# Performance work log

Measured on AMD Instinct MI355X. Metric: run time of the kernel, lower is better.

## Reference

```python
import jax, jax.numpy as jnp
from jax import lax
import numpy as np

# pywt sym4 analysis filters (pywt.Wavelet('sym4').dec_lo / .dec_hi)
DEC_LO = np.array([-0.07576571478927333, -0.02963552764599851, 0.49761866763201545,
                   0.8037387518059161, 0.29785779560527736, -0.09921954357684722,
                   -0.012603967262037833, 0.0322231006040427], dtype=np.float32)
DEC_HI = np.array([-0.0322231006040427, -0.012603967262037833, 0.09921954357684722,
                   0.29785779560527736, -0.8037387518059161, 0.49761866763201545,
                   0.02963552764599851, -0.07576571478927333], dtype=np.float32)
L = 8            # sym4 filter length
LEVEL = 4
THRESH = 10.0


def _conv1d(x, kernel, stride, pad):
    # x: (B, T), kernel: (L,) used in correlation sense by lax.conv
    y = lax.conv_general_dilated(x[:, None, :], kernel[None, None, :],
                                 window_strides=(stride,), padding=[pad],
                                 dimension_numbers=('NCH', 'OIH', 'NCH'))
    return y[:, 0, :]


def _dwt1(x, filt):
    # pywt single-level DWT, mode='symmetric':
    #   pad L-1 each side (half-sample symmetric), true convolution, take odd-index
    #   outputs of the 'valid' part -> length floor((N+L-1)/2)
    ext = jnp.pad(x, ((0, 0), (L - 1, L - 1)), mode='symmetric')[:, 1:]
    return _conv1d(ext, filt[::-1], 2, (0, 0))  # flip -> true convolution


def _idwt1(cA, cD, lo, hi):
    # pywt single-level IDWT: upsample by 2, full-convolve with rec filters, sum,
    # trim L-2 from the left, output length 2*n - L + 2.
    B, n = cA.shape
    upA = jnp.zeros((B, 2 * n), cA.dtype).at[:, ::2].set(cA)
    upD = jnp.zeros((B, 2 * n), cD.dtype).at[:, ::2].set(cD)
    # rec_lo = dec_lo[::-1]; full conv w/ rec_lo == correlation w/ dec_lo
    y = _conv1d(upA, lo, 1, (L - 1, L - 1)) + _conv1d(upD, hi, 1, (L - 1, L - 1))
    return y[:, L - 2: L - 2 + 2 * n - L + 2]


def _wavelet_denoise(x):
    lo = jnp.asarray(DEC_LO)
    hi = jnp.asarray(DEC_HI)
    a = x
    details = []
    for _ in range(LEVEL):
        details.append(_dwt1(a, hi))
        a = _dwt1(a, lo)
    # hard threshold: KEEP coefficients with |c| <= threshold, zero the rest
    details = [jnp.where(jnp.abs(d) <= THRESH, d, jnp.zeros_like(d)) for d in details]
    rec = a
    for d in reversed(details):
        if rec.shape[1] > d.shape[1]:     # pywt waverec a[:-1] trim
            rec = rec[:, :d.shape[1]]
        rec = _idwt1(rec, d, lo, hi)
    return rec


def setup_inputs() -> dict:
    key = jax.random.key(0)
    k1, k2 = jax.random.split(key)
    x = jax.random.normal(k1, (100000, 512), dtype=jnp.float32) * 20.0
    edge_index = jax.random.randint(k2, (2, 100000), 0, 100000, dtype=jnp.int64)
    return {"x": x, "edge_index": edge_index, "num_nodes": 100000}


def reference(x, edge_index, num_nodes):
    # edge_index / num_nodes are unused by the original forward
    return _wavelet_denoise(x)
```

## Files before the change

### kernel.cpp

```cpp
#include <hip/hip_runtime.h>
#include <cstddef>

#define THRESH_V 10.0f
#define RPB 4
#define SLICE 1040

static __device__ __forceinline__ void wave_sync() {
  asm volatile("s_waitcnt lgkmcnt(0)" ::: "memory");
}

#define RLO0 ( 0.0322231006040427f)
#define RLO1 (-0.012603967262037833f)
#define RLO2 (-0.09921954357684722f)
#define RLO3 ( 0.29785779560527736f)
#define RLO4 ( 0.8037387518059161f)
#define RLO5 ( 0.49761866763201545f)
#define RLO6 (-0.02963552764599851f)
#define RLO7 (-0.07576571478927333f)
#define RHI0 (-0.07576571478927333f)
#define RHI1 ( 0.02963552764599851f)
#define RHI2 ( 0.49761866763201545f)
#define RHI3 (-0.8037387518059161f)
#define RHI4 ( 0.29785779560527736f)
#define RHI5 ( 0.09921954357684722f)
#define RHI6 (-0.012603967262037833f)
#define RHI7 (-0.0322231006040427f)

static __device__ __forceinline__ float2 fwd_core(float v0, float v1, float v2,
                                                  float v3, float v4, float v5,
                                                  float v6, float v7) {
#pragma clang fp contract(off)
  float pl0 = v0 * RLO0, pl1 = v1 * RLO1, pl2 = v2 * RLO2, pl3 = v3 * RLO3;
  float pl4 = v4 * RLO4, pl5 = v5 * RLO5, pl6 = v6 * RLO6, pl7 = v7 * RLO7;
  float ph0 = v0 * RHI0, ph1 = v1 * RHI1, ph2 = v2 * RHI2, ph3 = v3 * RHI3;
  float ph4 = v4 * RHI4, ph5 = v5 * RHI5, ph6 = v6 * RHI6, ph7 = v7 * RHI7;
  float sLo = ((pl0 + pl1) + (pl2 + pl3)) + ((pl4 + pl5) + (pl6 + pl7));
  float sHi = ((ph0 + ph1) + (ph2 + ph3)) + ((ph4 + ph5) + (ph6 + ph7));
  return make_float2(sLo, sHi);
}

static __device__ __forceinline__ float symget(const float* E, const float* O,
                                               int k, int n) {
  int idx = (k < 0) ? (-1 - k) : ((k >= n) ? (2 * n - 1 - k) : k);
  return (idx & 1) ? O[idx >> 1] : E[idx >> 1];
}

template <bool SPLIT_OUT>
static __device__ __forceinline__ void fwd_stage(const float* __restrict__ E,
                                                 const float* __restrict__ O,
                                                 int n,
                                                 float* __restrict__ caE,
                                                 float* __restrict__ caO,
                                                 float* __restrict__ cd,
                                                 int lane) {
  const int m = (n + 7) >> 1;
  const int iMax = (n - 2) >> 1;

  for (int i = 3 + lane; i <= iMax; i += 64) {
    const float* e = E + (i - 3);
    const float* o = O + (i - 3);
    float2 s = fwd_core(e[0], o[0], e[1], o[1], e[2], o[2], e[3], o[3]);
    if constexpr (SPLIT_OUT) {
      float* dst = (i & 1) ? caO : caE;
      dst[i >> 1] = s.x;
    } else {
      caE[i] = s.x;
    }
    cd[i] = (fabsf(s.y) <= THRESH_V) ? s.y : 0.f;
  }

  int bi = -1;
  if (lane < 3) bi = lane;
  else if (lane >= 4 && lane < 8) {
    const int t = lane - 4;
    if (t < m - 1 - iMax) bi = iMax + 1 + t;
  }
  if (bi >= 0) {
    float v[8];
#pragma unroll
    for (int t = 0; t < 8; ++t) v[t] = symget(E, O, 2 * bi - 6 + t, n);
    float2 s = fwd_core(v[0], v[1], v[2], v[3], v[4], v[5], v[6], v[7]);
    if constexpr (SPLIT_OUT) {
      float* dst = (bi & 1) ? caO : caE;
      dst[bi >> 1] = s.x;
    } else {
      caE[bi] = s.x;
    }
    cd[bi] = (fabsf(s.y) <= THRESH_V) ? s.y : 0.f;
  }
}

static __device__ __forceinline__ void inv_stage(const float* __restrict__ ca,
                                                 const float* __restrict__ cd,
                                                 float* __restrict__ dst,
                                                 int outLen, int lane) {
  const int pairs = (outLen + 1) >> 1;
  for (int t = lane; t < pairs; t += 64) {
    float a0 = ca[t], a1 = ca[t + 1], a2 = ca[t + 2], a3 = ca[t + 3];
    float e0 = cd[t], e1 = cd[t + 1], e2 = cd[t + 2], e3 = cd[t + 3];
    float se = fmaf(a0, -0.02963552764599851f,
               fmaf(a1,  0.8037387518059161f,
               fmaf(a2, -0.09921954357684722f, a3 *  0.0322231006040427f)))
             + fmaf(e0, -0.012603967262037833f,
               fmaf(e1,  0.29785779560527736f,
               fmaf(e2,  0.49761866763201545f, e3 * -0.07576571478927333f)));
    float so = fmaf(a0, -0.07576571478927333f,
               fmaf(a1,  0.49761866763201545f,
               fmaf(a2,  0.29785779560527736f, a3 * -0.012603967262037833f)))
             + fmaf(e0, -0.0322231006040427f,
               fmaf(e1,  0.09921954357684722f,
               fmaf(e2, -0.8037387518059161f,  e3 *  0.02963552764599851f)));
    const int q = 2 * t;
    if (q + 1 < outLen) {
      *reinterpret_cast<float2*>(dst + q) = make_float2(se, so);
    } else {
      dst[q] = se;
    }
  }
}

__global__ __launch_bounds__(256, 8) void wavelet_denoise_kernel(
    const float* __restrict__ x, float* __restrict__ out, int nrows) {
  __shared__ float lds[RPB][SLICE];
  const int wave = threadIdx.x >> 6;
  const int lane = threadIdx.x & 63;
  const int row = blockIdx.x * RPB + wave;
  if (row >= nrows) return;

  float* S = lds[wave];
  float* sxE  = S;
  float* sxO  = S + 256;
  float* ca1E = S + 512;
  float* ca1O = S + 642;
  float* d1   = S + 772;
  float* ca2E = S + 0;
  float* ca2O = S + 67;
  float* d2   = S + 133;
  float* ca3E = S + 266;
  float* ca3O = S + 301;
  float* d3   = S + 336;
  float* ca4  = S + 406;
  float* d4   = S + 444;
  float* rec70  = S + 512;
  float* rec133 = S + 0;
  float* rec259 = S + 512;

  {
    const float4* src4 = reinterpret_cast<const float4*>(x + (size_t)row * 512);
    float2* dE = reinterpret_cast<float2*>(sxE);
    float2* dO = reinterpret_cast<float2*>(sxO);
    for (int c = lane; c < 128; c += 64) {
      float4 v = src4[c];
      dE[c] = make_float2(v.x, v.z);
      dO[c] = make_float2(v.y, v.w);
    }
  }
  wave_sync();

  fwd_stage<true >(sxE,  sxO,  512, ca1E, ca1O,   d1, lane); wave_sync();
  fwd_stage<true >(ca1E, ca1O, 259, ca2E, ca2O,   d2, lane); wave_sync();
  fwd_stage<true >(ca2E, ca2O, 133, ca3E, ca3O,   d3, lane); wave_sync();
  fwd_stage<false>(ca3E, ca3O,  70, ca4,  nullptr, d4, lane); wave_sync();

  inv_stage(ca4,    d4, rec70,   70, lane); wave_sync();
  inv_stage(rec70,  d3, rec133, 133, lane); wave_sync();
  inv_stage(rec133, d2, rec259, 259, lane); wave_sync();
  inv_stage(rec259, d1, out + (size_t)row * 512, 512, lane);
}

extern "C" void kernel_launch(void* const* d_in, const int* in_sizes, int n_in,
                              void* d_out, int out_size, void* d_ws, size_t ws_size,
                              hipStream_t stream) {
  const float* x = (const float*)d_in[0];
  float* out = (float*)d_out;
  const int nrows = in_sizes[0] / 512;
  const int grid = (nrows + RPB - 1) / RPB;
  wavelet_denoise_kernel<<<dim3(grid), dim3(256), 0, stream>>>(x, out, nrows);
}
```

Baseline: 382.7 us.

## Materialize symmetric padding in LDS and vectorize filter math with packed float2

Each forward stage now writes the symmetric boundary extension into LDS guard cells (fill_ext) before it runs. That lets one uniform loop cover all outputs and removes the separate boundary-lane path with its symget index logic. The filter arithmetic is rewritten with ext_vector float2 so the compiler can emit packed FP32 instructions, and LDS offsets are reshuffled to leave room for the guard cells. The cost is an extra fill pass and sync per stage, and the changed summation order and FMA contraction in the inverse stage may shift rounding slightly.

```diff
diff --git a/kernel.cpp b/kernel.cpp
--- a/kernel.cpp
+++ b/kernel.cpp
@@ -1,48 +1,44 @@
 #include <hip/hip_runtime.h>
 #include <cstddef>
 
+typedef float f2 __attribute__((ext_vector_type(2)));
+
 #define THRESH_V 10.0f
 #define RPB 4
-#define SLICE 1040
+#define SLICE 1064
 
 static __device__ __forceinline__ void wave_sync() {
   asm volatile("s_waitcnt lgkmcnt(0)" ::: "memory");
 }
 
-#define RLO0 ( 0.0322231006040427f)
-#define RLO1 (-0.012603967262037833f)
-#define RLO2 (-0.09921954357684722f)
-#define RLO3 ( 0.29785779560527736f)
-#define RLO4 ( 0.8037387518059161f)
-#define RLO5 ( 0.49761866763201545f)
-#define RLO6 (-0.02963552764599851f)
-#define RLO7 (-0.07576571478927333f)
-#define RHI0 (-0.07576571478927333f)
-#define RHI1 ( 0.02963552764599851f)
-#define RHI2 ( 0.49761866763201545f)
-#define RHI3 (-0.8037387518059161f)
-#define RHI4 ( 0.29785779560527736f)
-#define RHI5 ( 0.09921954357684722f)
-#define RHI6 (-0.012603967262037833f)
-#define RHI7 (-0.0322231006040427f)
+#define L0 (-0.07576571478927333f)
+#define L1 (-0.02963552764599851f)
+#define L2 ( 0.49761866763201545f)
+#define L3 ( 0.8037387518059161f)
+#define L4 ( 0.29785779560527736f)
+#define L5 (-0.09921954357684722f)
+#define L6 (-0.012603967262037833f)
+#define L7 ( 0.0322231006040427f)
+#define H0 (-0.0322231006040427f)
+#define H1 (-0.012603967262037833f)
+#define H2 ( 0.09921954357684722f)
+#define H3 ( 0.29785779560527736f)
+#define H4 (-0.8037387518059161f)
+#define H5 ( 0.49761866763201545f)
+#define H6 ( 0.02963552764599851f)
+#define H7 (-0.07576571478927333f)
 
-static __device__ __forceinline__ float2 fwd_core(float v0, float v1, float v2,
-                                                  float v3, float v4, float v5,
-                                                  float v6, float v7) {
-#pragma clang fp contract(off)
-  float pl0 = v0 * RLO0, pl1 = v1 * RLO1, pl2 = v2 * RLO2, pl3 = v3 * RLO3;
-  float pl4 = v4 * RLO4, pl5 = v5 * RLO5, pl6 = v6 * RLO6, pl7 = v7 * RLO7;
-  float ph0 = v0 * RHI0, ph1 = v1 * RHI1, ph2 = v2 * RHI2, ph3 = v3 * RHI3;
-  float ph4 = v4 * RHI4, ph5 = v5 * RHI5, ph6 = v6 * RHI6, ph7 = v7 * RHI7;
-  float sLo = ((pl0 + pl1) + (pl2 + pl3)) + ((pl4 + pl5) + (pl6 + pl7));
-  float sHi = ((ph0 + ph1) + (ph2 + ph3)) + ((ph4 + ph5) + (ph6 + ph7));
-  return make_float2(sLo, sHi);
-}
-
-static __device__ __forceinline__ float symget(const float* E, const float* O,
-                                               int k, int n) {
-  int idx = (k < 0) ? (-1 - k) : ((k >= n) ? (2 * n - 1 - k) : k);
-  return (idx & 1) ? O[idx >> 1] : E[idx >> 1];
+static __device__ __forceinline__ void fill_ext(float* E, float* O, int n, int lane) {
+  int k = 0;
+  bool act = false;
+  if (lane < 6)                      { k = -1 - lane;      act = true; }
+  else if (lane >= 8 && lane < 15)   { k = n + (lane - 8); act = true; }
+  if (act) {
+    const int src = (k < 0) ? (-1 - k) : (2 * n - 1 - k);
+    const float v = (src & 1) ? O[src >> 1] : E[src >> 1];
+    if (k & 1) O[(k - 1) >> 1] = v;
+    else       E[k >> 1] = v;
+  }
 }
 
 template <bool SPLIT_OUT>
@@ -53,40 +49,27 @@
                                                  float* __restrict__ caO,
                                                  float* __restrict__ cd,
                                                  int lane) {
+#pragma clang fp contract(off)
+  const f2 CLa = {L7, L5}, CLb = {L6, L4}, CLc = {L3, L1}, CLd = {L2, L0};
+  const f2 CHa = {H7, H5}, CHb = {H6, H4}, CHc = {H3, H1}, CHd = {H2, H0};
   const int m = (n + 7) >> 1;
-  const int iMax = (n - 2) >> 1;
-
-  for (int i = 3 + lane; i <= iMax; i += 64) {
-    const float* e = E + (i - 3);
-    const float* o = O + (i - 3);
-    float2 s = fwd_core(e[0], o[0], e[1], o[1], e[2], o[2], e[3], o[3]);
-    if constexpr (SPLIT_OUT) {
-      float* dst = (i & 1) ? caO : caE;
-      dst[i >> 1] = s.x;
-    } else {
-      caE[i] = s.x;
-    }
-    cd[i] = (fabsf(s.y) <= THRESH_V) ? s.y : 0.f;
-  }
-
-  int bi = -1;
-  if (lane < 3) bi = lane;
-  else if (lane >= 4 && lane < 8) {
-    const int t = lane - 4;
-    if (t < m - 1 - iMax) bi = iMax + 1 + t;
-  }
-  if (bi >= 0) {
-    float v[8];
-#pragma unroll
-    for (int t = 0; t < 8; ++t) v[t] = symget(E, O, 2 * bi - 6 + t, n);
-    float2 s = fwd_core(v[0], v[1], v[2], v[3], v[4], v[5], v[6], v[7]);
-    if constexpr (SPLIT_OUT) {
-      float* dst = (bi & 1) ? caO : caE;
-      dst[bi >> 1] = s.x;
-    } else {
-      caE[bi] = s.x;
-    }
-    cd[bi] = (fabsf(s.y) <= THRESH_V) ? s.y : 0.f;
+  float* const myCa = SPLIT_OUT ? ((lane & 1) ? caO : caE) : caE;
+  for (int i = lane; i < m; i += 64) {
+    const float* e = E + i - 3;
+    const float* o = O + i - 3;
+    f2 Ea; Ea.x = e[0]; Ea.y = e[1];
+    f2 Eb; Eb.x = e[2]; Eb.y = e[3];
+    f2 Oa; Oa.x = o[0]; Oa.y = o[1];
+    f2 Ob; Ob.x = o[2]; Ob.y = o[3];
+    f2 t1 = Ea * CLa + Oa * CLb;
+    f2 t2 = Eb * CLc + Ob * CLd;
+    const float sLo = (t1.x + t1.y) + (t2.x + t2.y);
+    f2 s1 = Ea * CHa + Oa * CHb;
+    f2 s2 = Eb * CHc + Ob * CHd;
+    const float sHi = (s1.x + s1.y) + (s2.x + s2.y);
+    if constexpr (SPLIT_OUT) myCa[i >> 1] = sLo;
+    else                     caE[i] = sLo;
+    cd[i] = (fabsf(sHi) <= THRESH_V) ? sHi : 0.f;
   }
 }
 
@@ -94,25 +77,23 @@
                                                  const float* __restrict__ cd,
                                                  float* __restrict__ dst,
                                                  int outLen, int lane) {
+#pragma clang fp contract(fast)
+  const f2 SEa = {L1, L3}, SEb = {L5, L7}, SEc = {H1, H3}, SEd = {H5, H7};
+  const f2 SOa = {L0, L2}, SOb = {L4, L6}, SOc = {H0, H2}, SOd = {H4, H6};
   const int pairs = (outLen + 1) >> 1;
   for (int t = lane; t < pairs; t += 64) {
-    float a0 = ca[t], a1 = ca[t + 1], a2 = ca[t + 2], a3 = ca[t + 3];
-    float e0 = cd[t], e1 = cd[t + 1], e2 = cd[t + 2], e3 = cd[t + 3];
-    float se = fmaf(a0, -0.02963552764599851f,
-               fmaf(a1,  0.8037387518059161f,
-               fmaf(a2, -0.09921954357684722f, a3 *  0.0322231006040427f)))
-             + fmaf(e0, -0.012603967262037833f,
-               fmaf(e1,  0.29785779560527736f,
-               fmaf(e2,  0.49761866763201545f, e3 * -0.07576571478927333f)));
-    float so = fmaf(a0, -0.07576571478927333f,
-               fmaf(a1,  0.49761866763201545f,
-               fmaf(a2,  0.29785779560527736f, a3 * -0.012603967262037833f)))
-             + fmaf(e0, -0.0322231006040427f,
-               fmaf(e1,  0.09921954357684722f,
-               fmaf(e2, -0.8037387518059161f,  e3 *  0.02963552764599851f)));
+    f2 a01; a01.x = ca[t];     a01.y = ca[t + 1];
+    f2 a23; a23.x = ca[t + 2]; a23.y = ca[t + 3];
+    f2 d01; d01.x = cd[t];     d01.y = cd[t + 1];
+    f2 d23; d23.x = cd[t + 2]; d23.y = cd[t + 3];
+    f2 mE = a01 * SEa + a23 * SEb + d01 * SEc + d23 * SEd;
+    f2 mO = a01 * SOa + a23 * SOb + d01 * SOc + d23 * SOd;
+    const float se = mE.x + mE.y;
+    const float so = mO.x + mO.y;
     const int q = 2 * t;
     if (q + 1 < outLen) {
-      *reinterpret_cast<float2*>(dst + q) = make_float2(se, so);
+      f2 r; r.x = se; r.y = so;
+      *reinterpret_cast<f2*>(dst + q) = r;
     } else {
       dst[q] = se;
     }
@@ -128,38 +109,40 @@
   if (row >= nrows) return;
 
   float* S = lds[wave];
-  float* sxE  = S;
-  float* sxO  = S + 256;
-  float* ca1E = S + 512;
-  float* ca1O = S + 642;
-  float* d1   = S + 772;
-  float* ca2E = S + 0;
-  float* ca2O = S + 67;
-  float* d2   = S + 133;
-  float* ca3E = S + 266;
-  float* ca3O = S + 301;
-  float* d3   = S + 336;
-  float* ca4  = S + 406;
-  float* d4   = S + 444;
-  float* rec70  = S + 512;
+  float* sxE  = S + 4;    float* sxO  = S + 268;
+  float* ca1E = S + 532;  float* ca1O = S + 670;
+  float* d1   = S + 804;
+  float* ca2E = S + 4;    float* ca2O = S + 78;
+  float* d2   = S + 148;
+  float* ca3E = S + 286;  float* ca3O = S + 330;
+  float* d3   = S + 368;
+  float* ca4  = S + 438;  float* d4   = S + 476;
+  float* rec70  = S + 528;
   float* rec133 = S + 0;
-  float* rec259 = S + 512;
+  float* rec259 = S + 528;
 
   {
     const float4* src4 = reinterpret_cast<const float4*>(x + (size_t)row * 512);
-    float2* dE = reinterpret_cast<float2*>(sxE);
-    float2* dO = reinterpret_cast<float2*>(sxO);
+    f2* dE = reinterpret_cast<f2*>(sxE);
+    f2* dO = reinterpret_cast<f2*>(sxO);
     for (int c = lane; c < 128; c += 64) {
       float4 v = src4[c];
-      dE[c] = make_float2(v.x, v.z);
-      dO[c] = make_float2(v.y, v.w);
+      f2 a; a.x = v.x; a.y = v.z;
+      f2 b; b.x = v.y; b.y = v.w;
+      dE[c] = a;
+      dO[c] = b;
     }
   }
   wave_sync();
+  fill_ext(sxE, sxO, 512, lane);
+  wave_sync();
 
   fwd_stage<true >(sxE,  sxO,  512, ca1E, ca1O,   d1, lane); wave_sync();
+  fill_ext(ca1E, ca1O, 259, lane);                           wave_sync();
   fwd_stage<true >(ca1E, ca1O, 259, ca2E, ca2O,   d2, lane); wave_sync();
+  fill_ext(ca2E, ca2O, 133, lane);                           wave_sync();
   fwd_stage<true >(ca2E, ca2O, 133, ca3E, ca3O,   d3, lane); wave_sync();
+  fill_ext(ca3E, ca3O, 70, lane);                            wave_sync();
   fwd_stage<false>(ca3E, ca3O,  70, ca4,  nullptr, d4, lane); wave_sync();
 
   inv_stage(ca4,    d4, rec70,   70, lane); wave_sync();
```

New measurement: 346.9 us. -9.4%, faster.
